# Kernel tuning notes

Measured on AMD Instinct MI355X. Metric: run time of the kernel, lower is better.

Reference implementation:

```python
import jax, jax.numpy as jnp
import numpy as np

N_NODES = 100000
N_EDGES = 1600000
N_GRAPHS = 64
EMB_DIM = 64
DIMS = [6, 16, 32, 64, EMB_DIM]


def setup_inputs() -> dict:
    key = jax.random.key(0)
    ks = jax.random.split(key, 16)
    feat = jax.random.normal(ks[0], (N_NODES, DIMS[0]), dtype=jnp.float32)
    src = jax.random.randint(ks[1], (N_EDGES,), 0, N_NODES)
    dst = jax.random.randint(ks[2], (N_EDGES,), 0, N_NODES)
    graph_ids = jnp.sort(jax.random.randint(ks[3], (N_NODES,), 0, N_GRAPHS))
    inp = {"feat": feat, "src": src, "dst": dst, "graph_ids": graph_ids}
    # fc_neigh weights for each SAGEConv (gcn aggregator has no fc_self), Xavier-ish init
    for i in range(4):
        din, dout = DIMS[i], DIMS[i + 1]
        scale = 1.0 / np.sqrt(din)
        inp[f"W{i+1}"] = jax.random.uniform(ks[4 + 2 * i], (din, dout), jnp.float32, -scale, scale)
        inp[f"b{i+1}"] = jnp.zeros((dout,), jnp.float32)
    return inp


def _sage_gcn(feat, src, dst, deg, W, b):
    # DGL SAGEConv aggregator_type='gcn':
    # h_neigh = (sum_{u in N(v)} h_u + h_v) / (in_deg(v) + 1); out = h_neigh @ W + b
    neigh = jax.ops.segment_sum(feat[src], dst, num_segments=N_NODES)  # [N, din]
    h = (neigh + feat) / (deg[:, None] + 1.0)
    return h @ W + b


def reference(feat, src, dst, graph_ids, W1, b1, W2, b2, W3, b3, W4, b4):
    deg = jax.ops.segment_sum(jnp.ones((N_EDGES,), feat.dtype), dst, num_segments=N_NODES)
    h = feat
    for W, b in ((W1, b1), (W2, b2), (W3, b3), (W4, b4)):
        h = jax.nn.relu(_sage_gcn(h, src, dst, deg, W, b))
    # dgl.mean_nodes: per-graph mean over nodes
    sums = jax.ops.segment_sum(h, graph_ids, num_segments=N_GRAPHS)          # [G, emb]
    cnts = jax.ops.segment_sum(jnp.ones((N_NODES,), h.dtype), graph_ids, num_segments=N_GRAPHS)
    return sums / jnp.maximum(cnts, 1.0)[:, None]
```

## Files before the change

### kernel.cpp

```cpp
#include <hip/hip_runtime.h>
#include <hip/hip_bf16.h>
#include <hip/hip_fp16.h>

#define N_NODES 100000
#define N_EDGES 1600000
#define N_GRAPHS 64

#define NB_BKT 256
#define NPBKT 391
#define EPB 1024
#define NBLK_BIN ((N_EDGES + EPB - 1) / EPB)


__device__ __forceinline__ __half2 u2h(unsigned int u) {
    return __builtin_bit_cast(__half2, u);
}
__device__ __forceinline__ float2 u2f2(unsigned int u) {
    return __half22float2(u2h(u));
}
__device__ __forceinline__ unsigned int packh2(float a, float b) {
    return __builtin_bit_cast(unsigned int, __float22half2_rn(make_float2(a, b)));
}


__global__ __launch_bounds__(256) void bin_count(const int* __restrict__ dst,
                                                 int* __restrict__ cntmat, int E) {
    __shared__ int cnt[NB_BKT];
    int t = threadIdx.x;
    int e0 = blockIdx.x * EPB;
    cnt[t] = 0;
    __syncthreads();
#pragma unroll
    for (int k = 0; k < 4; ++k) {
        int e = e0 + k * 256 + t;
        if (e < E) {
            unsigned d = (unsigned)dst[e];
            atomicAdd(&cnt[d / (unsigned)NPBKT], 1);
        }
    }
    __syncthreads();
    cntmat[(size_t)blockIdx.x * NB_BKT + t] = cnt[t];
}

__global__ __launch_bounds__(256) void bin_scan(int* __restrict__ cntmat,
                                                int* __restrict__ gcnt, int nblk) {
    __shared__ int s[256];
    int b = blockIdx.x, t = threadIdx.x;
    int running = 0;
    for (int c0 = 0; c0 < nblk; c0 += 256) {
        int idx = c0 + t;
        int v = (idx < nblk) ? cntmat[(size_t)idx * NB_BKT + b] : 0;
        s[t] = v;
        __syncthreads();
        for (int o = 1; o < 256; o <<= 1) {
            int a = (t >= o) ? s[t - o] : 0;
            __syncthreads();
            s[t] += a;
            __syncthreads();
        }
        if (idx < nblk) cntmat[(size_t)idx * NB_BKT + b] = running + s[t] - v;
        running += s[255];
        __syncthreads();
    }
    if (t == 0) gcnt[b] = running;
}

__global__ void scan256k(const int* __restrict__ gcnt, int* __restrict__ colbase) {
    __shared__ int s[256];
    int t = threadIdx.x;
    int c = gcnt[t];
    s[t] = c;
    __syncthreads();
    for (int o = 1; o < 256; o <<= 1) {
        int a = (t >= o) ? s[t - o] : 0;
        __syncthreads();
        s[t] += a;
        __syncthreads();
    }
    colbase[t] = s[t] - c;
    if (t == 255) colbase[256] = s[255];
}

__global__ __launch_bounds__(256) void bin_write(const int* __restrict__ dst,
                                                 const int* __restrict__ src,
                                                 const int* __restrict__ cntmat,
                                                 const int* __restrict__ colbase,
                                                 uint2* __restrict__ rec, int E) {
    __shared__ int cnt[NB_BKT];
    __shared__ int lbase[NB_BKT];
    __shared__ int gofs[NB_BKT];
    __shared__ uint2 stage[EPB];
    int t = threadIdx.x;
    int e0 = blockIdx.x * EPB;
    cnt[t] = 0;
    gofs[t] = colbase[t] + cntmat[(size_t)blockIdx.x * NB_BKT + t];
    __syncthreads();
    int myb[4], mypos[4];
    unsigned myd[4], mys[4];
#pragma unroll
    for (int k = 0; k < 4; ++k) {
        int e = e0 + k * 256 + t;
        if (e < E) {
            unsigned d = (unsigned)dst[e];
            int b = (int)(d / (unsigned)NPBKT);
            myd[k] = d;
            mys[k] = (unsigned)src[e];
            myb[k] = b;
            mypos[k] = atomicAdd(&cnt[b], 1);
        } else {
            myb[k] = -1;
        }
    }
    __syncthreads();
    int c = cnt[t];
    lbase[t] = c;
    __syncthreads();
    for (int o = 1; o < 256; o <<= 1) {
        int a = (t >= o) ? lbase[t - o] : 0;
        __syncthreads();
        lbase[t] += a;
        __syncthreads();
    }
    lbase[t] = lbase[t] - c;
    __syncthreads();
#pragma unroll
    for (int k = 0; k < 4; ++k)
        if (myb[k] >= 0) stage[lbase[myb[k]] + mypos[k]] = make_uint2(myd[k], mys[k]);
    __syncthreads();
    int total = min(EPB, E - e0);
    for (int i = t; i < total; i += 256) {
        int lo = 0, hi = NB_BKT - 1;
        while (lo < hi) {
            int m = (lo + hi + 1) >> 1;
            if (lbase[m] <= i) lo = m; else hi = m - 1;
        }
        rec[(size_t)gofs[lo] + (i - lbase[lo])] = stage[i];
    }
}

__global__ __launch_bounds__(256) void fill_bucket(const uint2* __restrict__ rec,
                                                   const int* __restrict__ colbase,
                                                   int* __restrict__ rp,
                                                   int* __restrict__ col, int n) {
    __shared__ int sdeg[512];
    __shared__ int lcur[512];
    __shared__ int lcol[8192];
    int p = blockIdx.x, t = threadIdx.x;
    int nbase = p * NPBKT;
    int nn = min(NPBKT, n - nbase);
    int cbase = colbase[p];
    int cnt = colbase[p + 1] - cbase;
    sdeg[t] = 0;
    sdeg[t + 256] = 0;
    __syncthreads();
    const uint2* r = rec + cbase;
    for (int i = t; i < cnt; i += 256) atomicAdd(&sdeg[r[i].x - (unsigned)nbase], 1);
    __syncthreads();
    int c0 = sdeg[t], c1 = sdeg[t + 256];
    for (int o = 1; o < 512; o <<= 1) {
        int a = (t >= o) ? sdeg[t - o] : 0;
        int b = (t + 256 >= o) ? sdeg[t + 256 - o] : 0;
        __syncthreads();
        sdeg[t] += a;
        sdeg[t + 256] += b;
        __syncthreads();
    }
    int ex0 = sdeg[t] - c0, ex1 = sdeg[t + 256] - c1;
    lcur[t] = ex0;
    lcur[t + 256] = ex1;
    if (t < nn) rp[nbase + t] = cbase + ex0;
    if (t + 256 < nn) rp[nbase + t + 256] = cbase + ex1;
    if (p == NB_BKT - 1 && t == 0) rp[n] = cbase + cnt;
    __syncthreads();
    for (int i = t; i < cnt; i += 256) {
        uint2 e = r[i];
        int slot = atomicAdd(&lcur[e.x - (unsigned)nbase], 1);
        lcol[slot] = (int)e.y;
    }
    __syncthreads();
    for (int i = t; i < cnt; i += 256) col[cbase + i] = lcol[i];
}


__global__ __launch_bounds__(256) void sage_layer1(const float* __restrict__ feat,
                                                   const int* __restrict__ rp,
                                                   const int* __restrict__ col,
                                                   const float* __restrict__ W,
                                                   const float* __restrict__ bias,
                                                   unsigned int* __restrict__ hout, int n) {
    __shared__ float sW[6 * 16];
    __shared__ float sB[16];
    int tid = threadIdx.x;
    if (tid < 96) sW[tid] = W[tid];
    if (tid < 16) sB[tid] = bias[tid];
    __syncthreads();
    int v = blockIdx.x * 256 + tid;
    if (v >= n) return;
    int r0 = rp[v], r1 = rp[v + 1];
    float acc[6] = {0.f, 0.f, 0.f, 0.f, 0.f, 0.f};
    const float2* f2 = reinterpret_cast<const float2*>(feat);
    int j = r0;
    for (; j + 4 <= r1; j += 4) {
        int u0 = col[j], u1 = col[j + 1], u2 = col[j + 2], u3 = col[j + 3];
        float2 a0 = f2[u0 * 3 + 0], b0 = f2[u0 * 3 + 1], c0 = f2[u0 * 3 + 2];
        float2 a1 = f2[u1 * 3 + 0], b1 = f2[u1 * 3 + 1], c1 = f2[u1 * 3 + 2];
        float2 a2 = f2[u2 * 3 + 0], b2 = f2[u2 * 3 + 1], c2 = f2[u2 * 3 + 2];
        float2 a3 = f2[u3 * 3 + 0], b3 = f2[u3 * 3 + 1], c3 = f2[u3 * 3 + 2];
        acc[0] += (a0.x + a1.x) + (a2.x + a3.x);
        acc[1] += (a0.y + a1.y) + (a2.y + a3.y);
        acc[2] += (b0.x + b1.x) + (b2.x + b3.x);
        acc[3] += (b0.y + b1.y) + (b2.y + b3.y);
        acc[4] += (c0.x + c1.x) + (c2.x + c3.x);
        acc[5] += (c0.y + c1.y) + (c2.y + c3.y);
    }
    for (; j < r1; ++j) {
        int u = col[j];
        float2 a = f2[u * 3 + 0], b = f2[u * 3 + 1], c = f2[u * 3 + 2];
        acc[0] += a.x; acc[1] += a.y;
        acc[2] += b.x; acc[3] += b.y;
        acc[4] += c.x; acc[5] += c.y;
    }
    {
        float2 a = f2[v * 3 + 0], b = f2[v * 3 + 1], c = f2[v * 3 + 2];
        acc[0] += a.x; acc[1] += a.y;
        acc[2] += b.x; acc[3] += b.y;
        acc[4] += c.x; acc[5] += c.y;
    }
    float inv = 1.0f / (float)(r1 - r0 + 1);
#pragma unroll
    for (int k = 0; k < 6; ++k) acc[k] *= inv;
    float outv[16];
#pragma unroll
    for (int o = 0; o < 16; ++o) outv[o] = sB[o];
#pragma unroll
    for (int k = 0; k < 6; ++k) {
#pragma unroll
        for (int o = 0; o < 16; ++o) outv[o] += acc[k] * sW[k * 16 + o];
    }
    unsigned int w[8];
#pragma unroll
    for (int o = 0; o < 16; o += 2)
        w[o / 2] = packh2(fmaxf(outv[o], 0.f), fmaxf(outv[o + 1], 0.f));
    uint4* op = reinterpret_cast<uint4*>(hout + v * 8);
    op[0] = make_uint4(w[0], w[1], w[2], w[3]);
    op[1] = make_uint4(w[4], w[5], w[6], w[7]);
}


template <int DIN, int DOUT>
__global__ __launch_bounds__(256) void sage_f16(const uint4* __restrict__ hin,
                                                const int* __restrict__ rp,
                                                const int* __restrict__ col,
                                                const float* __restrict__ W,
                                                const float* __restrict__ bias,
                                                unsigned int* __restrict__ hout, int n) {
    constexpr int WPN = DIN / 8;
    constexpr int NPB = 256 / WPN;
    constexpr int OPT = DOUT / WPN;
    __shared__ float sW[DIN * DOUT];
    __shared__ float sB[DOUT];
    __shared__ float sH[NPB][DIN + 1];

    int tid = threadIdx.x;
    for (int i = tid; i < DIN * DOUT; i += 256) sW[i] = W[i];
    if (tid < DOUT) sB[tid] = bias[tid];

    int sub = tid / WPN;
    int t = tid % WPN;
    int v = blockIdx.x * NPB + sub;

    if (v < n) {
        int r0 = rp[v], r1 = rp[v + 1];
        const __half2 z = __float2half2_rn(0.f);
        __half2 a0[4] = {z, z, z, z}, a1[4] = {z, z, z, z};
        __half2 a2[4] = {z, z, z, z}, a3[4] = {z, z, z, z};
        int j = r0;
        for (; j + 4 <= r1; j += 4) {
            int u0 = col[j], u1 = col[j + 1], u2 = col[j + 2], u3 = col[j + 3];
            uint4 w0 = hin[u0 * WPN + t];
            uint4 w1 = hin[u1 * WPN + t];
            uint4 w2 = hin[u2 * WPN + t];
            uint4 w3 = hin[u3 * WPN + t];
            a0[0] = __hadd2(a0[0], u2h(w0.x)); a0[1] = __hadd2(a0[1], u2h(w0.y));
            a0[2] = __hadd2(a0[2], u2h(w0.z)); a0[3] = __hadd2(a0[3], u2h(w0.w));
            a1[0] = __hadd2(a1[0], u2h(w1.x)); a1[1] = __hadd2(a1[1], u2h(w1.y));
            a1[2] = __hadd2(a1[2], u2h(w1.z)); a1[3] = __hadd2(a1[3], u2h(w1.w));
            a2[0] = __hadd2(a2[0], u2h(w2.x)); a2[1] = __hadd2(a2[1], u2h(w2.y));
            a2[2] = __hadd2(a2[2], u2h(w2.z)); a2[3] = __hadd2(a2[3], u2h(w2.w));
            a3[0] = __hadd2(a3[0], u2h(w3.x)); a3[1] = __hadd2(a3[1], u2h(w3.y));
            a3[2] = __hadd2(a3[2], u2h(w3.z)); a3[3] = __hadd2(a3[3], u2h(w3.w));
        }
        for (; j < r1; ++j) {
            uint4 w = hin[col[j] * WPN + t];
            a0[0] = __hadd2(a0[0], u2h(w.x)); a0[1] = __hadd2(a0[1], u2h(w.y));
            a0[2] = __hadd2(a0[2], u2h(w.z)); a0[3] = __hadd2(a0[3], u2h(w.w));
        }
#pragma unroll
        for (int q = 0; q < 4; ++q)
            a0[q] = __hadd2(__hadd2(a0[q], a1[q]), __hadd2(a2[q], a3[q]));
        uint4 ws = hin[v * WPN + t];
        unsigned swd[4] = {ws.x, ws.y, ws.z, ws.w};
        float inv = 1.0f / (float)(r1 - r0 + 1);
#pragma unroll
        for (int q = 0; q < 4; ++q) {
            float2 f = __half22float2(a0[q]);
            float2 s = u2f2(swd[q]);
            sH[sub][t * 8 + 2 * q + 0] = (f.x + s.x) * inv;
            sH[sub][t * 8 + 2 * q + 1] = (f.y + s.y) * inv;
        }
    }
    __syncthreads();
    if (v < n) {
        int o0 = t * OPT;
        float accO[OPT];
#pragma unroll
        for (int i = 0; i < OPT; ++i) accO[i] = sB[o0 + i];
#pragma unroll 4
        for (int k = 0; k < DIN; ++k) {
            float hk = sH[sub][k];
#pragma unroll
            for (int i = 0; i < OPT; ++i) accO[i] += hk * sW[k * DOUT + o0 + i];
        }
        unsigned wds[OPT / 2];
#pragma unroll
        for (int i = 0; i < OPT; i += 2)
            wds[i / 2] = packh2(fmaxf(accO[i], 0.f), fmaxf(accO[i + 1], 0.f));
        unsigned* op = hout + v * (DOUT / 2) + o0 / 2;
        if constexpr (OPT / 2 == 4) {
            *reinterpret_cast<uint4*>(op) = make_uint4(wds[0], wds[1], wds[2], wds[3]);
        } else if constexpr (OPT / 2 == 8) {
            reinterpret_cast<uint4*>(op)[0] = make_uint4(wds[0], wds[1], wds[2], wds[3]);
            reinterpret_cast<uint4*>(op)[1] = make_uint4(wds[4], wds[5], wds[6], wds[7]);
        } else {
            *reinterpret_cast<uint2*>(op) = make_uint2(wds[0], wds[1]);
        }
    }
}


__device__ __forceinline__ int lower_bound_i(const int* __restrict__ a, int n, int key) {
    int lo = 0, hi = n;
    while (lo < hi) {
        int m = (lo + hi) >> 1;
        if (a[m] < key) lo = m + 1; else hi = m;
    }
    return lo;
}

__global__ __launch_bounds__(256) void pool_f16(const unsigned int* __restrict__ h32,
                                                const int* __restrict__ gids,
                                                float* __restrict__ out, int n) {
    int bx = blockIdx.x;
    int g = bx >> 3, s = bx & 7;
    int start = lower_bound_i(gids, n, g);
    int end = lower_bound_i(gids, n, g + 1);
    int len = end - start;
    float inv = 1.0f / (float)(len > 0 ? len : 1);
    int chunk = (len + 7) / 8;
    int s0 = start + s * chunk;
    int s1 = min(s0 + chunk, end);
    int t = threadIdx.x;
    int d = t & 31, j = t >> 5;
    float a0 = 0.f, a1 = 0.f;
    for (int i = s0 + j; i < s1; i += 8) {
        float2 f = u2f2(h32[(size_t)i * 32 + d]);
        a0 += f.x;
        a1 += f.y;
    }
    __shared__ float red[8][32][2];
    red[j][d][0] = a0;
    red[j][d][1] = a1;
    __syncthreads();
    if (t < 64) {
        int dd = t & 31, e = t >> 5;
        float tot = 0.f;
#pragma unroll
        for (int k = 0; k < 8; ++k) tot += red[k][dd][e];
        atomicAdd(&out[g * 64 + 2 * dd + e], tot * inv);
    }
}


extern "C" void kernel_launch(void* const* d_in, const int* in_sizes, int n_in,
                              void* d_out, int out_size, void* d_ws, size_t ws_size,
                              hipStream_t stream) {
    const int N = N_NODES, E = N_EDGES;
    const float* feat = (const float*)d_in[0];
    const int* src = (const int*)d_in[1];
    const int* dst = (const int*)d_in[2];
    const int* gids = (const int*)d_in[3];
    const float* W1 = (const float*)d_in[4];
    const float* b1 = (const float*)d_in[5];
    const float* W2 = (const float*)d_in[6];
    const float* b2 = (const float*)d_in[7];
    const float* W3 = (const float*)d_in[8];
    const float* b3 = (const float*)d_in[9];
    const float* W4 = (const float*)d_in[10];
    const float* b4 = (const float*)d_in[11];
    float* out = (float*)d_out;

    int* rp = (int*)d_ws;
    int* gcnt = rp + (N + 1);
    int* colbase = gcnt + 256;
    int* cntmat = colbase + 257;
    int* col = cntmat + (size_t)NBLK_BIN * 256;
    size_t off = (size_t)((char*)(col + E) - (char*)d_ws);
    off = (off + 255) & ~(size_t)255;
    unsigned int* h1 = (unsigned int*)((char*)d_ws + off);
    unsigned int* h2 = h1 + (size_t)N * 8;
    unsigned int* h3 = h2 + (size_t)N * 16;
    unsigned int* h4 = h3 + (size_t)N * 32;
    uint2* rec = (uint2*)h3;

    hipMemsetAsync(out, 0, (size_t)N_GRAPHS * 64 * sizeof(float), stream);

    bin_count<<<NBLK_BIN, 256, 0, stream>>>(dst, cntmat, E);
    bin_scan<<<NB_BKT, 256, 0, stream>>>(cntmat, gcnt, NBLK_BIN);
    scan256k<<<1, 256, 0, stream>>>(gcnt, colbase);
    bin_write<<<NBLK_BIN, 256, 0, stream>>>(dst, src, cntmat, colbase, rec, E);
    fill_bucket<<<NB_BKT, 256, 0, stream>>>(rec, colbase, rp, col, N);

    sage_layer1<<<(N + 255) / 256, 256, 0, stream>>>(feat, rp, col, W1, b1, h1, N);
    sage_f16<16, 32><<<(N + 127) / 128, 256, 0, stream>>>(
        (const uint4*)h1, rp, col, W2, b2, h2, N);
    sage_f16<32, 64><<<(N + 63) / 64, 256, 0, stream>>>(
        (const uint4*)h2, rp, col, W3, b3, h3, N);
    sage_f16<64, 64><<<(N + 31) / 32, 256, 0, stream>>>(
        (const uint4*)h3, rp, col, W4, b4, h4, N);

    pool_f16<<<N_GRAPHS * 8, 256, 0, stream>>>(h4, gids, out, N);
}
```

Measured before the change: 183.2 us.

## Fold bucket-offset scan into consumers, double edges per bin block, widen gather unroll

Removes the single-block scan256k launch. bin_write and fill_bucket now each recompute the exclusive scan of bucket counts redundantly in shared memory. The edges handled per binning block double, which halves the block count and the size of the count matrix that bin_scan walks. The f16 SAGE gather loop is unrolled to 8 outstanding neighbor loads to raise memory-level parallelism, at the cost of more registers and extra per-block scan work.

```diff
diff --git a/kernel.cpp b/kernel.cpp
--- a/kernel.cpp
+++ b/kernel.cpp
@@ -8,7 +8,7 @@
 
 #define NB_BKT 256
 #define NPBKT 391
-#define EPB 1024
+#define EPB 2048
 #define NBLK_BIN ((N_EDGES + EPB - 1) / EPB)
 
 
@@ -31,7 +31,7 @@
     cnt[t] = 0;
     __syncthreads();
 #pragma unroll
-    for (int k = 0; k < 4; ++k) {
+    for (int k = 0; k < 8; ++k) {
         int e = e0 + k * 256 + t;
         if (e < E) {
             unsigned d = (unsigned)dst[e];
@@ -65,26 +65,10 @@
     if (t == 0) gcnt[b] = running;
 }
 
-__global__ void scan256k(const int* __restrict__ gcnt, int* __restrict__ colbase) {
-    __shared__ int s[256];
-    int t = threadIdx.x;
-    int c = gcnt[t];
-    s[t] = c;
-    __syncthreads();
-    for (int o = 1; o < 256; o <<= 1) {
-        int a = (t >= o) ? s[t - o] : 0;
-        __syncthreads();
-        s[t] += a;
-        __syncthreads();
-    }
-    colbase[t] = s[t] - c;
-    if (t == 255) colbase[256] = s[255];
-}
-
 __global__ __launch_bounds__(256) void bin_write(const int* __restrict__ dst,
                                                  const int* __restrict__ src,
                                                  const int* __restrict__ cntmat,
-                                                 const int* __restrict__ colbase,
+                                                 const int* __restrict__ gcnt,
                                                  uint2* __restrict__ rec, int E) {
     __shared__ int cnt[NB_BKT];
     __shared__ int lbase[NB_BKT];
@@ -92,13 +76,22 @@
     __shared__ uint2 stage[EPB];
     int t = threadIdx.x;
     int e0 = blockIdx.x * EPB;
+    int g = gcnt[t];
+    lbase[t] = g;
+    __syncthreads();
+    for (int o = 1; o < 256; o <<= 1) {
+        int a = (t >= o) ? lbase[t - o] : 0;
+        __syncthreads();
+        lbase[t] += a;
+        __syncthreads();
+    }
+    gofs[t] = (lbase[t] - g) + cntmat[(size_t)blockIdx.x * NB_BKT + t];
     cnt[t] = 0;
-    gofs[t] = colbase[t] + cntmat[(size_t)blockIdx.x * NB_BKT + t];
-    __syncthreads();
-    int myb[4], mypos[4];
-    unsigned myd[4], mys[4];
-#pragma unroll
-    for (int k = 0; k < 4; ++k) {
+    __syncthreads();
+    int myb[8], mypos[8];
+    unsigned myd[8], mys[8];
+#pragma unroll
+    for (int k = 0; k < 8; ++k) {
         int e = e0 + k * 256 + t;
         if (e < E) {
             unsigned d = (unsigned)dst[e];
@@ -124,7 +117,7 @@
     lbase[t] = lbase[t] - c;
     __syncthreads();
 #pragma unroll
-    for (int k = 0; k < 4; ++k)
+    for (int k = 0; k < 8; ++k)
         if (myb[k] >= 0) stage[lbase[myb[k]] + mypos[k]] = make_uint2(myd[k], mys[k]);
     __syncthreads();
     int total = min(EPB, E - e0);
@@ -139,17 +132,31 @@
 }
 
 __global__ __launch_bounds__(256) void fill_bucket(const uint2* __restrict__ rec,
-                                                   const int* __restrict__ colbase,
+                                                   const int* __restrict__ gcnt,
                                                    int* __restrict__ rp,
                                                    int* __restrict__ col, int n) {
     __shared__ int sdeg[512];
     __shared__ int lcur[512];
+    __shared__ int sg[256];
     __shared__ int lcol[8192];
     int p = blockIdx.x, t = threadIdx.x;
     int nbase = p * NPBKT;
     int nn = min(NPBKT, n - nbase);
-    int cbase = colbase[p];
-    int cnt = colbase[p + 1] - cbase;
+    int g = gcnt[t];
+    sg[t] = g;
+    __syncthreads();
+    for (int o = 1; o < 256; o <<= 1) {
+        int a = (t >= o) ? sg[t - o] : 0;
+        __syncthreads();
+        sg[t] += a;
+        __syncthreads();
+    }
+    int ex = sg[t] - g;
+    __syncthreads();
+    sg[t] = ex;
+    __syncthreads();
+    int cbase = sg[p];
+    int cnt = gcnt[p];
     sdeg[t] = 0;
     sdeg[t + 256] = 0;
     __syncthreads();
@@ -272,38 +279,55 @@
     if (v < n) {
         int r0 = rp[v], r1 = rp[v + 1];
         const __half2 z = __float2half2_rn(0.f);
-        __half2 a0[4] = {z, z, z, z}, a1[4] = {z, z, z, z};
-        __half2 a2[4] = {z, z, z, z}, a3[4] = {z, z, z, z};
+        __half2 acc[4][4];
+#pragma unroll
+        for (int s = 0; s < 4; ++s)
+#pragma unroll
+            for (int q = 0; q < 4; ++q) acc[s][q] = z;
         int j = r0;
+        for (; j + 8 <= r1; j += 8) {
+            uint4 w[8];
+#pragma unroll
+            for (int k = 0; k < 8; ++k) w[k] = hin[col[j + k] * WPN + t];
+#pragma unroll
+            for (int k = 0; k < 8; ++k) {
+                __half2* a = acc[k & 3];
+                a[0] = __hadd2(a[0], u2h(w[k].x));
+                a[1] = __hadd2(a[1], u2h(w[k].y));
+                a[2] = __hadd2(a[2], u2h(w[k].z));
+                a[3] = __hadd2(a[3], u2h(w[k].w));
+            }
+        }
         for (; j + 4 <= r1; j += 4) {
-            int u0 = col[j], u1 = col[j + 1], u2 = col[j + 2], u3 = col[j + 3];
-            uint4 w0 = hin[u0 * WPN + t];
-            uint4 w1 = hin[u1 * WPN + t];
-            uint4 w2 = hin[u2 * WPN + t];
-            uint4 w3 = hin[u3 * WPN + t];
-            a0[0] = __hadd2(a0[0], u2h(w0.x)); a0[1] = __hadd2(a0[1], u2h(w0.y));
-            a0[2] = __hadd2(a0[2], u2h(w0.z)); a0[3] = __hadd2(a0[3], u2h(w0.w));
-            a1[0] = __hadd2(a1[0], u2h(w1.x)); a1[1] = __hadd2(a1[1], u2h(w1.y));
-            a1[2] = __hadd2(a1[2], u2h(w1.z)); a1[3] = __hadd2(a1[3], u2h(w1.w));
-            a2[0] = __hadd2(a2[0], u2h(w2.x)); a2[1] = __hadd2(a2[1], u2h(w2.y));
-            a2[2] = __hadd2(a2[2], u2h(w2.z)); a2[3] = __hadd2(a2[3], u2h(w2.w));
-            a3[0] = __hadd2(a3[0], u2h(w3.x)); a3[1] = __hadd2(a3[1], u2h(w3.y));
-            a3[2] = __hadd2(a3[2], u2h(w3.z)); a3[3] = __hadd2(a3[3], u2h(w3.w));
+            uint4 w[4];
+#pragma unroll
+            for (int k = 0; k < 4; ++k) w[k] = hin[col[j + k] * WPN + t];
+#pragma unroll
+            for (int k = 0; k < 4; ++k) {
+                __half2* a = acc[k];
+                a[0] = __hadd2(a[0], u2h(w[k].x));
+                a[1] = __hadd2(a[1], u2h(w[k].y));
+                a[2] = __hadd2(a[2], u2h(w[k].z));
+                a[3] = __hadd2(a[3], u2h(w[k].w));
+            }
         }
         for (; j < r1; ++j) {
             uint4 w = hin[col[j] * WPN + t];
-            a0[0] = __hadd2(a0[0], u2h(w.x)); a0[1] = __hadd2(a0[1], u2h(w.y));
-            a0[2] = __hadd2(a0[2], u2h(w.z)); a0[3] = __hadd2(a0[3], u2h(w.w));
+            acc[0][0] = __hadd2(acc[0][0], u2h(w.x));
+            acc[0][1] = __hadd2(acc[0][1], u2h(w.y));
+            acc[0][2] = __hadd2(acc[0][2], u2h(w.z));
+            acc[0][3] = __hadd2(acc[0][3], u2h(w.w));
         }
 #pragma unroll
         for (int q = 0; q < 4; ++q)
-            a0[q] = __hadd2(__hadd2(a0[q], a1[q]), __hadd2(a2[q], a3[q]));
+            acc[0][q] = __hadd2(__hadd2(acc[0][q], acc[1][q]),
+                                __hadd2(acc[2][q], acc[3][q]));
         uint4 ws = hin[v * WPN + t];
         unsigned swd[4] = {ws.x, ws.y, ws.z, ws.w};
         float inv = 1.0f / (float)(r1 - r0 + 1);
 #pragma unroll
         for (int q = 0; q < 4; ++q) {
-            float2 f = __half22float2(a0[q]);
+            float2 f = __half22float2(acc[0][q]);
             float2 s = u2f2(swd[q]);
             sH[sub][t * 8 + 2 * q + 0] = (f.x + s.x) * inv;
             sH[sub][t * 8 + 2 * q + 1] = (f.y + s.y) * inv;
@@ -401,8 +425,7 @@
 
     int* rp = (int*)d_ws;
     int* gcnt = rp + (N + 1);
-    int* colbase = gcnt + 256;
-    int* cntmat = colbase + 257;
+    int* cntmat = gcnt + 256;
     int* col = cntmat + (size_t)NBLK_BIN * 256;
     size_t off = (size_t)((char*)(col + E) - (char*)d_ws);
     off = (off + 255) & ~(size_t)255;
@@ -416,9 +439,8 @@
 
     bin_count<<<NBLK_BIN, 256, 0, stream>>>(dst, cntmat, E);
     bin_scan<<<NB_BKT, 256, 0, stream>>>(cntmat, gcnt, NBLK_BIN);
-    scan256k<<<1, 256, 0, stream>>>(gcnt, colbase);
-    bin_write<<<NBLK_BIN, 256, 0, stream>>>(dst, src, cntmat, colbase, rec, E);
-    fill_bucket<<<NB_BKT, 256, 0, stream>>>(rec, colbase, rp, col, N);
+    bin_write<<<NBLK_BIN, 256, 0, stream>>>(dst, src, cntmat, gcnt, rec, E);
+    fill_bucket<<<NB_BKT, 256, 0, stream>>>(rec, gcnt, rp, col, N);
 
     sage_layer1<<<(N + 255) / 256, 256, 0, stream>>>(feat, rp, col, W1, b1, h1, N);
     sage_f16<16, 32><<<(N + 127) / 128, 256, 0, stream>>>(
```

After: 176.8 us. 3.5% less time.
